# Kernel tuning notes

Hardware: AMD Instinct MI355X
Metric: run time of the kernel (lower is better)

Reference implementation:

```python
import jax, jax.numpy as jnp
import numpy as np

N_NODES = 50000
N_EDGES = 800000
HIDDEN = 128
NUM_GDL = 2


def setup_inputs() -> dict:
    key = jax.random.key(0)
    k0, k1, k2, k3, k4 = jax.random.split(key, 5)
    x = jax.random.normal(k0, (N_NODES, HIDDEN), dtype=jnp.float32)
    row = jax.random.randint(k1, (N_EDGES,), 0, N_NODES, dtype=jnp.int32)
    # ensure every node appears at least once as a target so degree >= 1
    col_tail = jax.random.randint(k2, (N_EDGES - N_NODES,), 0, N_NODES, dtype=jnp.int32)
    col = jnp.concatenate([jnp.arange(N_NODES, dtype=jnp.int32), col_tail])
    edge_index = jnp.stack([row, col], axis=0)  # [2, E]
    W1s = jax.random.normal(k3, (NUM_GDL, HIDDEN, HIDDEN), dtype=jnp.float32) / np.sqrt(HIDDEN).astype(np.float32)
    W2s = jax.random.normal(k4, (NUM_GDL, HIDDEN, 2 * HIDDEN), dtype=jnp.float32) / np.sqrt(2 * HIDDEN).astype(np.float32)
    biases = jnp.zeros((NUM_GDL, HIDDEN), dtype=jnp.float32)  # reset_parameters zeroes bias
    return {"x": x, "edge_index": edge_index, "W1s": W1s, "W2s": W2s, "biases": biases}


def reference(x, edge_index, W1s, W2s, biases):
    # eval mode: dropout is identity
    row, col = edge_index[0], edge_index[1]  # row = source j, col = target i
    n, d = x.shape
    deg = jax.ops.segment_sum(jnp.ones(row.shape[0], x.dtype), col, num_segments=n)
    norm = (1.0 / deg)[row]  # per-edge norm, indexed by row as in torch source
    for k in range(W1s.shape[0]):
        W1, W2, b = W1s[k], W2s[k], biases[k]
        # lin2(cat[x_i, x_j]) = x_i @ W2[:, :d].T + x_j @ W2[:, d:].T
        # precompute both node-level projections, then gather per edge (cheaper than per-edge GEMM)
        proj_i = x @ W2[:, :d].T  # [n, d]
        proj_j = x @ W2[:, d:].T  # [n, d]
        msg = norm[:, None] * (proj_i[col] + proj_j[row])  # [E, d]
        agg = jax.ops.segment_sum(msg, col, num_segments=n)  # scatter-add into targets
        out = x @ W1.T - agg + b
        x = jax.nn.gelu(out, approximate=False)  # torch nn.GELU default = exact erf
    return x
```

## Files before the change

### kernel.cpp

```cpp
#include <hip/hip_runtime.h>

#define N_NODES 50000
#define N_EDGES 800000
#define D 128
#define NBUCKET 196
#define CAP 8192
#define EPT 16
#define SCAT_BLOCKS 196
#define WCONV_BLOCKS 96
#define CAST_BLOCKS 6250
#define GEMM_TILES 391

typedef unsigned short ushort_t;
typedef __bf16 bf16x8 __attribute__((ext_vector_type(8)));
typedef float f32x4 __attribute__((ext_vector_type(4)));
typedef float f32x2 __attribute__((ext_vector_type(2)));

__device__ __forceinline__ ushort_t f2bf(float f) {
    unsigned u = __builtin_bit_cast(unsigned, f);
    u += 0x7FFFu + ((u >> 16) & 1u);
    return (ushort_t)(u >> 16);
}
__device__ __forceinline__ float bf2f(unsigned h16) {
    return __builtin_bit_cast(float, h16 << 16);
}

__global__ __launch_bounds__(256) void k_pre(const float* __restrict__ x, ushort_t* __restrict__ xb,
                                             const int* __restrict__ row, const int* __restrict__ col,
                                             int* __restrict__ bucket_cursor, int2* __restrict__ temp,
                                             const float* __restrict__ W1s, const float* __restrict__ W2s,
                                             ushort_t* __restrict__ Wb) {
    __shared__ int hist[NBUCKET];
    int b = blockIdx.x;
    if (b < SCAT_BLOCKS) {
        for (int t = threadIdx.x; t < NBUCKET; t += 256) hist[t] = 0;
        __syncthreads();
        int base = (b * 256 + threadIdx.x) * EPT;
        bool act = base < N_EDGES;
        int4 c[4], r[4];
        if (act) {
            #pragma unroll
            for (int q = 0; q < 4; ++q) c[q] = *(const int4*)(col + base + q * 4);
            #pragma unroll
            for (int q = 0; q < 4; ++q) r[q] = *(const int4*)(row + base + q * 4);
            #pragma unroll
            for (int q = 0; q < 4; ++q) {
                atomicAdd(&hist[c[q].x >> 8], 1); atomicAdd(&hist[c[q].y >> 8], 1);
                atomicAdd(&hist[c[q].z >> 8], 1); atomicAdd(&hist[c[q].w >> 8], 1);
            }
        }
        __syncthreads();
        for (int t = threadIdx.x; t < NBUCKET; t += 256) {
            int cnt = hist[t];
            hist[t] = cnt ? atomicAdd(&bucket_cursor[t], cnt) : 0;
        }
        __syncthreads();
        if (act) {
            #pragma unroll
            for (int q = 0; q < 4; ++q) {
                int cc[4] = { c[q].x, c[q].y, c[q].z, c[q].w };
                int rr[4] = { r[q].x, r[q].y, r[q].z, r[q].w };
                #pragma unroll
                for (int e = 0; e < 4; ++e) {
                    int bk = cc[e] >> 8;
                    int pos = atomicAdd(&hist[bk], 1);
                    temp[bk * CAP + pos] = make_int2(rr[e], cc[e]);
                }
            }
        }
    } else if (b < SCAT_BLOCKS + WCONV_BLOCKS) {
        int c = (b - SCAT_BLOCKS) * 256 + threadIdx.x;
        int k = c / 12288, rem = c % 12288;
        int mat = rem / 4096, rr = (rem % 4096) / 32, col4 = rem % 32;
        const float* src = (mat == 0)
            ? (W1s + k * 16384 + rr * 128 + col4 * 4)
            : (W2s + k * 32768 + rr * 256 + (mat == 2 ? 128 : 0) + col4 * 4);
        float4 v = *(const float4*)src;
        ushort_t tmp[4] = { f2bf(v.x), f2bf(v.y), f2bf(v.z), f2bf(v.w) };
        *(uint2*)(Wb + ((size_t)(k * 3 + mat)) * 16384 + rr * 128 + col4 * 4) = *(const uint2*)tmp;
    } else {
        int base = ((b - SCAT_BLOCKS - WCONV_BLOCKS) * 256 + threadIdx.x) * 4;
        if (base < N_NODES * D) {
            float4 v = *(const float4*)(x + base);
            ushort_t tmp[4] = { f2bf(v.x), f2bf(v.y), f2bf(v.z), f2bf(v.w) };
            *(uint2*)(xb + base) = *(const uint2*)tmp;
        }
    }
}

__device__ __forceinline__ void gemm_tile3(int m0,
                                           ushort_t (*As)[136], ushort_t (*Bs)[136],
                                           const ushort_t* __restrict__ xb,
                                           const ushort_t* __restrict__ Wl,
                                           const float* __restrict__ scl,
                                           ushort_t* __restrict__ Plb,
                                           ushort_t* __restrict__ Pi_,
                                           unsigned char* __restrict__ Pj8) {
    const int tid = threadIdx.x;
    #pragma unroll
    for (int it = 0; it < 8; ++it) {
        int c = tid + it * 256;
        int r = c >> 4, kc = c & 15;
        uint4 v = make_uint4(0, 0, 0, 0);
        int gm = m0 + r;
        if (gm < N_NODES) v = *(const uint4*)(xb + (size_t)gm * D + kc * 8);
        *(uint4*)&As[r][kc * 8] = v;
    }
    const int w = tid >> 6, lane = tid & 63, quad = lane >> 4, r16 = lane & 15;
    const int arow0 = w * 32 + r16, arow1 = arow0 + 16;
    #pragma unroll
    for (int y = 0; y < 3; ++y) {
        const ushort_t* Wmat = Wl + (size_t)y * 16384;
        #pragma unroll
        for (int it = 0; it < 8; ++it) {
            int c = tid + it * 256;
            int r = c >> 4, kc = c & 15;
            *(uint4*)&Bs[r][kc * 8] = *(const uint4*)(Wmat + r * 128 + kc * 8);
        }
        __syncthreads();
        f32x4 acc[2][8];
        #pragma unroll
        for (int mt = 0; mt < 2; ++mt)
            #pragma unroll
            for (int nt = 0; nt < 8; ++nt) acc[mt][nt] = (f32x4){0.f, 0.f, 0.f, 0.f};
        #pragma unroll
        for (int k0 = 0; k0 < 128; k0 += 32) {
            bf16x8 a0 = __builtin_bit_cast(bf16x8, *(const uint4*)&As[arow0][k0 + quad * 8]);
            bf16x8 a1 = __builtin_bit_cast(bf16x8, *(const uint4*)&As[arow1][k0 + quad * 8]);
            #pragma unroll
            for (int nt = 0; nt < 8; ++nt) {
                bf16x8 b = __builtin_bit_cast(bf16x8, *(const uint4*)&Bs[nt * 16 + r16][k0 + quad * 8]);
                acc[0][nt] = __builtin_amdgcn_mfma_f32_16x16x32_bf16(b, a0, acc[0][nt], 0, 0, 0);
                acc[1][nt] = __builtin_amdgcn_mfma_f32_16x16x32_bf16(b, a1, acc[1][nt], 0, 0, 0);
            }
        }
        #pragma unroll
        for (int mt = 0; mt < 2; ++mt) {
            int gm = m0 + w * 32 + mt * 16 + r16;
            if (gm >= N_NODES) continue;
            if (y < 2) {
                ushort_t* Outp = (y == 0) ? Plb : Pi_;
                #pragma unroll
                for (int nt = 0; nt < 8; ++nt) {
                    ushort_t tmp[4] = { f2bf(acc[mt][nt][0]), f2bf(acc[mt][nt][1]),
                                        f2bf(acc[mt][nt][2]), f2bf(acc[mt][nt][3]) };
                    *(uint2*)(Outp + (size_t)gm * D + nt * 16 + quad * 4) = *(const uint2*)tmp;
                }
            } else {
                float sc = scl ? scl[gm] : 1.0f;
                #pragma unroll
                for (int nt = 0; nt < 8; ++nt) {
                    int v = __builtin_amdgcn_cvt_pk_fp8_f32(acc[mt][nt][0] * sc, acc[mt][nt][1] * sc, 0, false);
                    v = __builtin_amdgcn_cvt_pk_fp8_f32(acc[mt][nt][2] * sc, acc[mt][nt][3] * sc, v, true);
                    *(unsigned*)(Pj8 + (size_t)gm * D + nt * 16 + quad * 4) = (unsigned)v;
                }
            }
        }
        if (y < 2) __syncthreads();
    }
}

__global__ __launch_bounds__(256) void k_bsort_gemm(const int2* __restrict__ temp,
                                                    const int* __restrict__ bucket_cursor,
                                                    int* __restrict__ csr, int* __restrict__ off,
                                                    int* __restrict__ deg, float* __restrict__ inv_deg,
                                                    const ushort_t* __restrict__ xb,
                                                    const ushort_t* __restrict__ Wb,
                                                    ushort_t* __restrict__ Plb,
                                                    ushort_t* __restrict__ Pi_,
                                                    unsigned char* __restrict__ Pj8) {
    __shared__ __align__(16) ushort_t As[128][136];
    __shared__ __align__(16) ushort_t Bs[128][136];
    __shared__ int hist[256];
    __shared__ int sm[256];
    if (blockIdx.x < NBUCKET) {
        int b = blockIdx.x, t = threadIdx.x;
        int cnt = bucket_cursor[b];
        sm[t] = (t < b) ? bucket_cursor[t] : 0;
        __syncthreads();
        for (int o = 1; o < 256; o <<= 1) {
            int add = (t >= o) ? sm[t - o] : 0;
            __syncthreads();
            sm[t] += add;
            __syncthreads();
        }
        int gbase = sm[255];
        int tbase = b * CAP;
        hist[t] = 0;
        __syncthreads();
        int i = t;
        for (; i + 768 < cnt; i += 1024) {
            int2 e0 = temp[tbase + i], e1 = temp[tbase + i + 256];
            int2 e2 = temp[tbase + i + 512], e3 = temp[tbase + i + 768];
            atomicAdd(&hist[e0.y & 255], 1); atomicAdd(&hist[e1.y & 255], 1);
            atomicAdd(&hist[e2.y & 255], 1); atomicAdd(&hist[e3.y & 255], 1);
        }
        for (; i < cnt; i += 256) atomicAdd(&hist[temp[tbase + i].y & 255], 1);
        __syncthreads();
        int c = hist[t];
        sm[t] = c;
        __syncthreads();
        for (int o = 1; o < 256; o <<= 1) {
            int add = (t >= o) ? sm[t - o] : 0;
            __syncthreads();
            sm[t] += add;
            __syncthreads();
        }
        int excl = sm[t] - c;
        int node = b * 256 + t;
        if (node < N_NODES) {
            off[node] = gbase + excl;
            deg[node] = c;
            inv_deg[node] = 1.0f / (float)c;
        }
        __syncthreads();
        hist[t] = gbase + excl;
        __syncthreads();
        i = t;
        for (; i + 768 < cnt; i += 1024) {
            int2 e0 = temp[tbase + i], e1 = temp[tbase + i + 256];
            int2 e2 = temp[tbase + i + 512], e3 = temp[tbase + i + 768];
            int p0 = atomicAdd(&hist[e0.y & 255], 1);
            int p1 = atomicAdd(&hist[e1.y & 255], 1);
            int p2 = atomicAdd(&hist[e2.y & 255], 1);
            int p3 = atomicAdd(&hist[e3.y & 255], 1);
            csr[p0] = e0.x; csr[p1] = e1.x; csr[p2] = e2.x; csr[p3] = e3.x;
        }
        for (; i < cnt; i += 256) {
            int2 e = temp[tbase + i];
            int p = atomicAdd(&hist[e.y & 255], 1);
            csr[p] = e.x;
        }
    } else {
        gemm_tile3((blockIdx.x - NBUCKET) * 128, As, Bs, xb, Wb, nullptr, Plb, Pi_, Pj8);
    }
}

__global__ __launch_bounds__(256) void k_gemm(const ushort_t* __restrict__ xb,
                                              const ushort_t* __restrict__ Wl,
                                              const float* __restrict__ inv_deg,
                                              ushort_t* __restrict__ Plb,
                                              ushort_t* __restrict__ Pi_,
                                              unsigned char* __restrict__ Pj8) {
    __shared__ __align__(16) ushort_t As[128][136];
    __shared__ __align__(16) ushort_t Bs[128][136];
    gemm_tile3(blockIdx.x * 128, As, Bs, xb, Wl, inv_deg, Plb, Pi_, Pj8);
}

__global__ __launch_bounds__(256) void k_agg(const ushort_t* __restrict__ Plb,
                                             const ushort_t* __restrict__ Pi_,
                                             const unsigned char* __restrict__ Pj8,
                                             const int* __restrict__ off,
                                             const int* __restrict__ deg,
                                             const int* __restrict__ csr,
                                             const float* __restrict__ inv_deg,
                                             const float* __restrict__ bias,
                                             float* __restrict__ s_arr,
                                             float* __restrict__ out_f32,
                                             ushort_t* __restrict__ out_bf16,
                                             int layer0) {
    int wv = __builtin_amdgcn_readfirstlane(threadIdx.x >> 6);
    int node = blockIdx.x * 4 + wv;
    if (node >= N_NODES) return;
    int lane = threadIdx.x & 63;
    unsigned ulin = *(const unsigned*)(Plb + (size_t)node * D + 2 * lane);
    unsigned upi  = *(const unsigned*)(Pi_ + (size_t)node * D + 2 * lane);
    float2 bv = *(const float2*)(bias + 2 * lane);
    float a0 = bf2f(ulin & 0xffffu) + bv.x;
    float a1 = bf2f(ulin >> 16)     + bv.y;
    float c0 = 0.f, c1 = 0.f, si;
    int e0 = off[node], ne = deg[node];
    int j = 0;
    if (layer0) {
        float sa = 0.f, sb = 0.f;
        for (; j + 16 <= ne; j += 16) {
            int sx[16];
            #pragma unroll
            for (int t = 0; t < 16; ++t) sx[t] = csr[e0 + j + t];
            unsigned u[16];
            #pragma unroll
            for (int t = 0; t < 16; ++t) u[t] = *(const ushort_t*)(Pj8 + (size_t)sx[t] * D + 2 * lane);
            float dv[16];
            #pragma unroll
            for (int t = 0; t < 16; ++t) dv[t] = inv_deg[sx[t]];
            #pragma unroll
            for (int t = 0; t < 16; t += 2) {
                f32x2 f0 = __builtin_amdgcn_cvt_pk_f32_fp8((int)u[t], false);
                f32x2 f1 = __builtin_amdgcn_cvt_pk_f32_fp8((int)u[t + 1], false);
                sa += dv[t]; sb += dv[t + 1];
                a0 -= dv[t] * f0[0];  c0 += dv[t + 1] * f1[0];
                a1 -= dv[t] * f0[1];  c1 += dv[t + 1] * f1[1];
            }
        }
        for (; j + 4 <= ne; j += 4) {
            int s0 = csr[e0 + j], s1 = csr[e0 + j + 1], s2 = csr[e0 + j + 2], s3 = csr[e0 + j + 3];
            unsigned u0 = *(const ushort_t*)(Pj8 + (size_t)s0 * D + 2 * lane);
            unsigned u1 = *(const ushort_t*)(Pj8 + (size_t)s1 * D + 2 * lane);
            unsigned u2 = *(const ushort_t*)(Pj8 + (size_t)s2 * D + 2 * lane);
            unsigned u3 = *(const ushort_t*)(Pj8 + (size_t)s3 * D + 2 * lane);
            float d0 = inv_deg[s0], d1 = inv_deg[s1], d2 = inv_deg[s2], d3 = inv_deg[s3];
            f32x2 f0 = __builtin_amdgcn_cvt_pk_f32_fp8((int)u0, false);
            f32x2 f1 = __builtin_amdgcn_cvt_pk_f32_fp8((int)u1, false);
            f32x2 f2 = __builtin_amdgcn_cvt_pk_f32_fp8((int)u2, false);
            f32x2 f3 = __builtin_amdgcn_cvt_pk_f32_fp8((int)u3, false);
            sa += d0 + d2; sb += d1 + d3;
            a0 -= d0 * f0[0] + d1 * f1[0];  c0 += d2 * f2[0] + d3 * f3[0];
            a1 -= d0 * f0[1] + d1 * f1[1];  c1 += d2 * f2[1] + d3 * f3[1];
        }
        for (; j < ne; ++j) {
            int s0 = csr[e0 + j];
            unsigned u0 = *(const ushort_t*)(Pj8 + (size_t)s0 * D + 2 * lane);
            float d0 = inv_deg[s0];
            f32x2 f0 = __builtin_amdgcn_cvt_pk_f32_fp8((int)u0, false);
            sa += d0;
            a0 -= d0 * f0[0];
            a1 -= d0 * f0[1];
        }
        si = sa + sb;
        if (lane == 0) s_arr[node] = si;
    } else {
        si = s_arr[node];
        for (; j + 16 <= ne; j += 16) {
            int sx[16];
            #pragma unroll
            for (int t = 0; t < 16; ++t) sx[t] = csr[e0 + j + t];
            unsigned u[16];
            #pragma unroll
            for (int t = 0; t < 16; ++t) u[t] = *(const ushort_t*)(Pj8 + (size_t)sx[t] * D + 2 * lane);
            #pragma unroll
            for (int t = 0; t < 16; t += 2) {
                f32x2 f0 = __builtin_amdgcn_cvt_pk_f32_fp8((int)u[t], false);
                f32x2 f1 = __builtin_amdgcn_cvt_pk_f32_fp8((int)u[t + 1], false);
                a0 -= f0[0];  c0 += f1[0];
                a1 -= f0[1];  c1 += f1[1];
            }
        }
        for (; j + 4 <= ne; j += 4) {
            int s0 = csr[e0 + j], s1 = csr[e0 + j + 1], s2 = csr[e0 + j + 2], s3 = csr[e0 + j + 3];
            unsigned u0 = *(const ushort_t*)(Pj8 + (size_t)s0 * D + 2 * lane);
            unsigned u1 = *(const ushort_t*)(Pj8 + (size_t)s1 * D + 2 * lane);
            unsigned u2 = *(const ushort_t*)(Pj8 + (size_t)s2 * D + 2 * lane);
            unsigned u3 = *(const ushort_t*)(Pj8 + (size_t)s3 * D + 2 * lane);
            f32x2 f0 = __builtin_amdgcn_cvt_pk_f32_fp8((int)u0, false);
            f32x2 f1 = __builtin_amdgcn_cvt_pk_f32_fp8((int)u1, false);
            f32x2 f2 = __builtin_amdgcn_cvt_pk_f32_fp8((int)u2, false);
            f32x2 f3 = __builtin_amdgcn_cvt_pk_f32_fp8((int)u3, false);
            a0 -= f0[0] + f1[0];  c0 += f2[0] + f3[0];
            a1 -= f0[1] + f1[1];  c1 += f2[1] + f3[1];
        }
        for (; j < ne; ++j) {
            int s0 = csr[e0 + j];
            unsigned u0 = *(const ushort_t*)(Pj8 + (size_t)s0 * D + 2 * lane);
            f32x2 f0 = __builtin_amdgcn_cvt_pk_f32_fp8((int)u0, false);
            a0 -= f0[0];
            a1 -= f0[1];
        }
    }
    a0 -= c0 + si * bf2f(upi & 0xffffu);
    a1 -= c1 + si * bf2f(upi >> 16);
    float g0 = 0.5f * a0 * (1.0f + erff(a0 * 0.70710678118654752440f));
    float g1 = 0.5f * a1 * (1.0f + erff(a1 * 0.70710678118654752440f));
    if (layer0) {
        ushort_t tmp[2] = { f2bf(g0), f2bf(g1) };
        *(unsigned*)(out_bf16 + (size_t)node * D + 2 * lane) = *(const unsigned*)tmp;
    } else {
        *(float2*)(out_f32 + (size_t)node * D + 2 * lane) = make_float2(g0, g1);
    }
}

extern "C" void kernel_launch(void* const* d_in, const int* in_sizes, int n_in,
                              void* d_out, int out_size, void* d_ws, size_t ws_size,
                              hipStream_t stream) {
    const float* x      = (const float*)d_in[0];
    const int*   ei     = (const int*)d_in[1];
    const int*   rowp   = ei;
    const int*   colp   = ei + N_EDGES;
    const float* W1s    = (const float*)d_in[2];
    const float* W2s    = (const float*)d_in[3];
    const float* biases = (const float*)d_in[4];
    float* out = (float*)d_out;

    char* ws = (char*)d_ws;
    size_t o = 0;
    auto carve = [&](size_t bytes) -> void* {
        void* p = ws + o;
        o = (o + bytes + 255) & ~(size_t)255;
        return p;
    };
    int*           bucket_cursor = (int*)carve(NBUCKET * 4);
    int*           deg     = (int*)carve(N_NODES * 4);
    float*         inv_deg = (float*)carve(N_NODES * 4);
    int*           off     = (int*)carve(N_NODES * 4);
    float*         s_arr   = (float*)carve(N_NODES * 4);
    int*           csr     = (int*)carve(N_EDGES * 4);
    int2*          temp    = (int2*)carve((size_t)NBUCKET * CAP * 8);
    ushort_t*      xb      = (ushort_t*)carve((size_t)N_NODES * D * 2);
    ushort_t*      Wb      = (ushort_t*)carve((size_t)2 * 3 * 16384 * 2);
    ushort_t*      Plb     = (ushort_t*)carve((size_t)N_NODES * D * 2);
    ushort_t*      Pi_     = (ushort_t*)carve((size_t)N_NODES * D * 2);
    unsigned char* Pj8     = (unsigned char*)carve((size_t)N_NODES * D);
    if (o > ws_size) return;

    hipMemsetAsync(bucket_cursor, 0, NBUCKET * 4, stream);

    k_pre<<<SCAT_BLOCKS + WCONV_BLOCKS + CAST_BLOCKS, 256, 0, stream>>>(x, xb, rowp, colp,
                                                                        bucket_cursor, temp,
                                                                        W1s, W2s, Wb);
    k_bsort_gemm<<<NBUCKET + GEMM_TILES, 256, 0, stream>>>(temp, bucket_cursor, csr, off,
                                                           deg, inv_deg, xb, Wb, Plb, Pi_, Pj8);

    const int AB = (N_NODES + 3) / 4;
    k_agg<<<AB, 256, 0, stream>>>(Plb, Pi_, Pj8, off, deg, csr, inv_deg, biases, s_arr,
                                  nullptr, xb, 1);
    k_gemm<<<GEMM_TILES, 256, 0, stream>>>(xb, Wb + (size_t)3 * 16384, inv_deg, Plb, Pi_, Pj8);
    k_agg<<<AB, 256, 0, stream>>>(Plb, Pi_, Pj8, off, deg, csr, inv_deg, biases + 128, s_arr,
                                  out, nullptr, 0);
}
```

Measured before the change: 206.1 us.

## Fuse x cast into GEMM, shrink CSR to 16-bit, widen agg gathers

```diff
diff --git a/kernel.cpp b/kernel.cpp
--- a/kernel.cpp
+++ b/kernel.cpp
@@ -8,7 +8,6 @@
 #define EPT 16
 #define SCAT_BLOCKS 196
 #define WCONV_BLOCKS 96
-#define CAST_BLOCKS 6250
 #define GEMM_TILES 391
 
 typedef unsigned short ushort_t;
@@ -25,9 +24,8 @@
     return __builtin_bit_cast(float, h16 << 16);
 }
 
-__global__ __launch_bounds__(256) void k_pre(const float* __restrict__ x, ushort_t* __restrict__ xb,
-                                             const int* __restrict__ row, const int* __restrict__ col,
-                                             int* __restrict__ bucket_cursor, int2* __restrict__ temp,
+__global__ __launch_bounds__(256) void k_pre(const int* __restrict__ row, const int* __restrict__ col,
+                                             int* __restrict__ bucket_cursor, unsigned* __restrict__ temp,
                                              const float* __restrict__ W1s, const float* __restrict__ W2s,
                                              ushort_t* __restrict__ Wb) {
     __shared__ int hist[NBUCKET];
@@ -64,11 +62,11 @@
                 for (int e = 0; e < 4; ++e) {
                     int bk = cc[e] >> 8;
                     int pos = atomicAdd(&hist[bk], 1);
-                    temp[bk * CAP + pos] = make_int2(rr[e], cc[e]);
+                    temp[bk * CAP + pos] = (unsigned)rr[e] | ((unsigned)(cc[e] & 255) << 16);
                 }
             }
         }
-    } else if (b < SCAT_BLOCKS + WCONV_BLOCKS) {
+    } else {
         int c = (b - SCAT_BLOCKS) * 256 + threadIdx.x;
         int k = c / 12288, rem = c % 12288;
         int mat = rem / 4096, rr = (rem % 4096) / 32, col4 = rem % 32;
@@ -78,33 +76,48 @@
         float4 v = *(const float4*)src;
         ushort_t tmp[4] = { f2bf(v.x), f2bf(v.y), f2bf(v.z), f2bf(v.w) };
         *(uint2*)(Wb + ((size_t)(k * 3 + mat)) * 16384 + rr * 128 + col4 * 4) = *(const uint2*)tmp;
-    } else {
-        int base = ((b - SCAT_BLOCKS - WCONV_BLOCKS) * 256 + threadIdx.x) * 4;
-        if (base < N_NODES * D) {
-            float4 v = *(const float4*)(x + base);
-            ushort_t tmp[4] = { f2bf(v.x), f2bf(v.y), f2bf(v.z), f2bf(v.w) };
-            *(uint2*)(xb + base) = *(const uint2*)tmp;
-        }
-    }
-}
-
+    }
+}
+
+template<bool AF32>
 __device__ __forceinline__ void gemm_tile3(int m0,
                                            ushort_t (*As)[136], ushort_t (*Bs)[136],
-                                           const ushort_t* __restrict__ xb,
+                                           const void* __restrict__ xsrc,
                                            const ushort_t* __restrict__ Wl,
                                            const float* __restrict__ scl,
                                            ushort_t* __restrict__ Plb,
                                            ushort_t* __restrict__ Pi_,
                                            unsigned char* __restrict__ Pj8) {
     const int tid = threadIdx.x;
-    #pragma unroll
-    for (int it = 0; it < 8; ++it) {
-        int c = tid + it * 256;
-        int r = c >> 4, kc = c & 15;
-        uint4 v = make_uint4(0, 0, 0, 0);
-        int gm = m0 + r;
-        if (gm < N_NODES) v = *(const uint4*)(xb + (size_t)gm * D + kc * 8);
-        *(uint4*)&As[r][kc * 8] = v;
+    if constexpr (AF32) {
+        const float* xf = (const float*)xsrc;
+        #pragma unroll
+        for (int it = 0; it < 8; ++it) {
+            int c = tid + it * 256;
+            int r = c >> 4, kc = c & 15;
+            uint4 v = make_uint4(0, 0, 0, 0);
+            int gm = m0 + r;
+            if (gm < N_NODES) {
+                float4 p0 = *(const float4*)(xf + (size_t)gm * D + kc * 8);
+                float4 p1 = *(const float4*)(xf + (size_t)gm * D + kc * 8 + 4);
+                ushort_t __attribute__((aligned(16))) tmp[8] =
+                    { f2bf(p0.x), f2bf(p0.y), f2bf(p0.z), f2bf(p0.w),
+                      f2bf(p1.x), f2bf(p1.y), f2bf(p1.z), f2bf(p1.w) };
+                v = *(const uint4*)tmp;
+            }
+            *(uint4*)&As[r][kc * 8] = v;
+        }
+    } else {
+        const ushort_t* xb = (const ushort_t*)xsrc;
+        #pragma unroll
+        for (int it = 0; it < 8; ++it) {
+            int c = tid + it * 256;
+            int r = c >> 4, kc = c & 15;
+            uint4 v = make_uint4(0, 0, 0, 0);
+            int gm = m0 + r;
+            if (gm < N_NODES) v = *(const uint4*)(xb + (size_t)gm * D + kc * 8);
+            *(uint4*)&As[r][kc * 8] = v;
+        }
     }
     const int w = tid >> 6, lane = tid & 63, quad = lane >> 4, r16 = lane & 15;
     const int arow0 = w * 32 + r16, arow1 = arow0 + 16;
@@ -160,11 +173,11 @@
     }
 }
 
-__global__ __launch_bounds__(256) void k_bsort_gemm(const int2* __restrict__ temp,
+__global__ __launch_bounds__(256) void k_bsort_gemm(const unsigned* __restrict__ temp,
                                                     const int* __restrict__ bucket_cursor,
-                                                    int* __restrict__ csr, int* __restrict__ off,
+                                                    ushort_t* __restrict__ csr, int* __restrict__ off,
                                                     int* __restrict__ deg, float* __restrict__ inv_deg,
-                                                    const ushort_t* __restrict__ xb,
+                                                    const float* __restrict__ xf,
                                                     const ushort_t* __restrict__ Wb,
                                                     ushort_t* __restrict__ Plb,
                                                     ushort_t* __restrict__ Pi_,
@@ -190,12 +203,12 @@
         __syncthreads();
         int i = t;
         for (; i + 768 < cnt; i += 1024) {
-            int2 e0 = temp[tbase + i], e1 = temp[tbase + i + 256];
-            int2 e2 = temp[tbase + i + 512], e3 = temp[tbase + i + 768];
-            atomicAdd(&hist[e0.y & 255], 1); atomicAdd(&hist[e1.y & 255], 1);
-            atomicAdd(&hist[e2.y & 255], 1); atomicAdd(&hist[e3.y & 255], 1);
-        }
-        for (; i < cnt; i += 256) atomicAdd(&hist[temp[tbase + i].y & 255], 1);
+            unsigned e0 = temp[tbase + i], e1 = temp[tbase + i + 256];
+            unsigned e2 = temp[tbase + i + 512], e3 = temp[tbase + i + 768];
+            atomicAdd(&hist[e0 >> 16], 1); atomicAdd(&hist[e1 >> 16], 1);
+            atomicAdd(&hist[e2 >> 16], 1); atomicAdd(&hist[e3 >> 16], 1);
+        }
+        for (; i < cnt; i += 256) atomicAdd(&hist[temp[tbase + i] >> 16], 1);
         __syncthreads();
         int c = hist[t];
         sm[t] = c;
@@ -218,21 +231,22 @@
         __syncthreads();
         i = t;
         for (; i + 768 < cnt; i += 1024) {
-            int2 e0 = temp[tbase + i], e1 = temp[tbase + i + 256];
-            int2 e2 = temp[tbase + i + 512], e3 = temp[tbase + i + 768];
-            int p0 = atomicAdd(&hist[e0.y & 255], 1);
-            int p1 = atomicAdd(&hist[e1.y & 255], 1);
-            int p2 = atomicAdd(&hist[e2.y & 255], 1);
-            int p3 = atomicAdd(&hist[e3.y & 255], 1);
-            csr[p0] = e0.x; csr[p1] = e1.x; csr[p2] = e2.x; csr[p3] = e3.x;
+            unsigned e0 = temp[tbase + i], e1 = temp[tbase + i + 256];
+            unsigned e2 = temp[tbase + i + 512], e3 = temp[tbase + i + 768];
+            int p0 = atomicAdd(&hist[e0 >> 16], 1);
+            int p1 = atomicAdd(&hist[e1 >> 16], 1);
+            int p2 = atomicAdd(&hist[e2 >> 16], 1);
+            int p3 = atomicAdd(&hist[e3 >> 16], 1);
+            csr[p0] = (ushort_t)e0; csr[p1] = (ushort_t)e1;
+            csr[p2] = (ushort_t)e2; csr[p3] = (ushort_t)e3;
         }
         for (; i < cnt; i += 256) {
-            int2 e = temp[tbase + i];
-            int p = atomicAdd(&hist[e.y & 255], 1);
-            csr[p] = e.x;
-        }
-    } else {
-        gemm_tile3((blockIdx.x - NBUCKET) * 128, As, Bs, xb, Wb, nullptr, Plb, Pi_, Pj8);
+            unsigned e = temp[tbase + i];
+            int p = atomicAdd(&hist[e >> 16], 1);
+            csr[p] = (ushort_t)e;
+        }
+    } else {
+        gemm_tile3<true>((blockIdx.x - NBUCKET) * 128, As, Bs, xf, Wb, nullptr, Plb, Pi_, Pj8);
     }
 }
 
@@ -244,7 +258,7 @@
                                               unsigned char* __restrict__ Pj8) {
     __shared__ __align__(16) ushort_t As[128][136];
     __shared__ __align__(16) ushort_t Bs[128][136];
-    gemm_tile3(blockIdx.x * 128, As, Bs, xb, Wl, inv_deg, Plb, Pi_, Pj8);
+    gemm_tile3<false>(blockIdx.x * 128, As, Bs, xb, Wl, inv_deg, Plb, Pi_, Pj8);
 }
 
 __global__ __launch_bounds__(256) void k_agg(const ushort_t* __restrict__ Plb,
@@ -252,7 +266,7 @@
                                              const unsigned char* __restrict__ Pj8,
                                              const int* __restrict__ off,
                                              const int* __restrict__ deg,
-                                             const int* __restrict__ csr,
+                                             const ushort_t* __restrict__ csr,
                                              const float* __restrict__ inv_deg,
                                              const float* __restrict__ bias,
                                              float* __restrict__ s_arr,
@@ -262,109 +276,146 @@
     int wv = __builtin_amdgcn_readfirstlane(threadIdx.x >> 6);
     int node = blockIdx.x * 4 + wv;
     if (node >= N_NODES) return;
-    int lane = threadIdx.x & 63;
-    unsigned ulin = *(const unsigned*)(Plb + (size_t)node * D + 2 * lane);
-    unsigned upi  = *(const unsigned*)(Pi_ + (size_t)node * D + 2 * lane);
-    float2 bv = *(const float2*)(bias + 2 * lane);
-    float a0 = bf2f(ulin & 0xffffu) + bv.x;
-    float a1 = bf2f(ulin >> 16)     + bv.y;
-    float c0 = 0.f, c1 = 0.f, si;
-    int e0 = off[node], ne = deg[node];
+    const int lane = threadIdx.x & 63;
+    const int g = lane >> 4;
+    const int q8 = lane & 15;
+    const int eoff = 8 * q8 + 2 * g;
+    unsigned ulin = *(const unsigned*)(Plb + (size_t)node * D + eoff);
+    unsigned upi  = *(const unsigned*)(Pi_ + (size_t)node * D + eoff);
+    float2 bv = *(const float2*)(bias + eoff);
+    float su[8];
+    #pragma unroll
+    for (int k = 0; k < 8; ++k) su[k] = 0.f;
+    float sd = 0.f;
+    const int e0 = off[node], ne = deg[node];
     int j = 0;
     if (layer0) {
-        float sa = 0.f, sb = 0.f;
         for (; j + 16 <= ne; j += 16) {
-            int sx[16];
-            #pragma unroll
-            for (int t = 0; t < 16; ++t) sx[t] = csr[e0 + j + t];
-            unsigned u[16];
-            #pragma unroll
-            for (int t = 0; t < 16; ++t) u[t] = *(const ushort_t*)(Pj8 + (size_t)sx[t] * D + 2 * lane);
-            float dv[16];
-            #pragma unroll
-            for (int t = 0; t < 16; ++t) dv[t] = inv_deg[sx[t]];
-            #pragma unroll
-            for (int t = 0; t < 16; t += 2) {
-                f32x2 f0 = __builtin_amdgcn_cvt_pk_f32_fp8((int)u[t], false);
-                f32x2 f1 = __builtin_amdgcn_cvt_pk_f32_fp8((int)u[t + 1], false);
-                sa += dv[t]; sb += dv[t + 1];
-                a0 -= dv[t] * f0[0];  c0 += dv[t + 1] * f1[0];
-                a1 -= dv[t] * f0[1];  c1 += dv[t + 1] * f1[1];
+            int sx[4];
+            #pragma unroll
+            for (int t = 0; t < 4; ++t) sx[t] = csr[e0 + j + 4 * t + g];
+            uint2 u[4];
+            #pragma unroll
+            for (int t = 0; t < 4; ++t) u[t] = *(const uint2*)(Pj8 + (size_t)sx[t] * D + 8 * q8);
+            float dv[4];
+            #pragma unroll
+            for (int t = 0; t < 4; ++t) dv[t] = inv_deg[sx[t]];
+            #pragma unroll
+            for (int t = 0; t < 4; ++t) {
+                f32x2 f0 = __builtin_amdgcn_cvt_pk_f32_fp8((int)u[t].x, false);
+                f32x2 f1 = __builtin_amdgcn_cvt_pk_f32_fp8((int)u[t].x, true);
+                f32x2 f2 = __builtin_amdgcn_cvt_pk_f32_fp8((int)u[t].y, false);
+                f32x2 f3 = __builtin_amdgcn_cvt_pk_f32_fp8((int)u[t].y, true);
+                sd += dv[t];
+                su[0] += dv[t] * f0[0]; su[1] += dv[t] * f0[1];
+                su[2] += dv[t] * f1[0]; su[3] += dv[t] * f1[1];
+                su[4] += dv[t] * f2[0]; su[5] += dv[t] * f2[1];
+                su[6] += dv[t] * f3[0]; su[7] += dv[t] * f3[1];
             }
         }
         for (; j + 4 <= ne; j += 4) {
-            int s0 = csr[e0 + j], s1 = csr[e0 + j + 1], s2 = csr[e0 + j + 2], s3 = csr[e0 + j + 3];
-            unsigned u0 = *(const ushort_t*)(Pj8 + (size_t)s0 * D + 2 * lane);
-            unsigned u1 = *(const ushort_t*)(Pj8 + (size_t)s1 * D + 2 * lane);
-            unsigned u2 = *(const ushort_t*)(Pj8 + (size_t)s2 * D + 2 * lane);
-            unsigned u3 = *(const ushort_t*)(Pj8 + (size_t)s3 * D + 2 * lane);
-            float d0 = inv_deg[s0], d1 = inv_deg[s1], d2 = inv_deg[s2], d3 = inv_deg[s3];
-            f32x2 f0 = __builtin_amdgcn_cvt_pk_f32_fp8((int)u0, false);
-            f32x2 f1 = __builtin_amdgcn_cvt_pk_f32_fp8((int)u1, false);
-            f32x2 f2 = __builtin_amdgcn_cvt_pk_f32_fp8((int)u2, false);
-            f32x2 f3 = __builtin_amdgcn_cvt_pk_f32_fp8((int)u3, false);
-            sa += d0 + d2; sb += d1 + d3;
-            a0 -= d0 * f0[0] + d1 * f1[0];  c0 += d2 * f2[0] + d3 * f3[0];
-            a1 -= d0 * f0[1] + d1 * f1[1];  c1 += d2 * f2[1] + d3 * f3[1];
-        }
-        for (; j < ne; ++j) {
-            int s0 = csr[e0 + j];
-            unsigned u0 = *(const ushort_t*)(Pj8 + (size_t)s0 * D + 2 * lane);
-            float d0 = inv_deg[s0];
-            f32x2 f0 = __builtin_amdgcn_cvt_pk_f32_fp8((int)u0, false);
-            sa += d0;
-            a0 -= d0 * f0[0];
-            a1 -= d0 * f0[1];
-        }
-        si = sa + sb;
+            int sx = csr[e0 + j + g];
+            uint2 u = *(const uint2*)(Pj8 + (size_t)sx * D + 8 * q8);
+            float dv = inv_deg[sx];
+            f32x2 f0 = __builtin_amdgcn_cvt_pk_f32_fp8((int)u.x, false);
+            f32x2 f1 = __builtin_amdgcn_cvt_pk_f32_fp8((int)u.x, true);
+            f32x2 f2 = __builtin_amdgcn_cvt_pk_f32_fp8((int)u.y, false);
+            f32x2 f3 = __builtin_amdgcn_cvt_pk_f32_fp8((int)u.y, true);
+            sd += dv;
+            su[0] += dv * f0[0]; su[1] += dv * f0[1];
+            su[2] += dv * f1[0]; su[3] += dv * f1[1];
+            su[4] += dv * f2[0]; su[5] += dv * f2[1];
+            su[6] += dv * f3[0]; su[7] += dv * f3[1];
+        }
+        if (j < ne) {
+            int r = ne - j;
+            int gi = (g < r) ? g : (r - 1);
+            int sx = csr[e0 + j + gi];
+            uint2 u = *(const uint2*)(Pj8 + (size_t)sx * D + 8 * q8);
+            float dv = (g < r) ? inv_deg[sx] : 0.f;
+            f32x2 f0 = __builtin_amdgcn_cvt_pk_f32_fp8((int)u.x, false);
+            f32x2 f1 = __builtin_amdgcn_cvt_pk_f32_fp8((int)u.x, true);
+            f32x2 f2 = __builtin_amdgcn_cvt_pk_f32_fp8((int)u.y, false);
+            f32x2 f3 = __builtin_amdgcn_cvt_pk_f32_fp8((int)u.y, true);
+            sd += dv;
+            su[0] += dv * f0[0]; su[1] += dv * f0[1];
+            su[2] += dv * f1[0]; su[3] += dv * f1[1];
+            su[4] += dv * f2[0]; su[5] += dv * f2[1];
+            su[6] += dv * f3[0]; su[7] += dv * f3[1];
+        }
+    } else {
+        for (; j + 16 <= ne; j += 16) {
+            int sx[4];
+            #pragma unroll
+            for (int t = 0; t < 4; ++t) sx[t] = csr[e0 + j + 4 * t + g];
+            uint2 u[4];
+            #pragma unroll
+            for (int t = 0; t < 4; ++t) u[t] = *(const uint2*)(Pj8 + (size_t)sx[t] * D + 8 * q8);
+            #pragma unroll
+            for (int t = 0; t < 4; ++t) {
+                f32x2 f0 = __builtin_amdgcn_cvt_pk_f32_fp8((int)u[t].x, false);
+                f32x2 f1 = __builtin_amdgcn_cvt_pk_f32_fp8((int)u[t].x, true);
+                f32x2 f2 = __builtin_amdgcn_cvt_pk_f32_fp8((int)u[t].y, false);
+                f32x2 f3 = __builtin_amdgcn_cvt_pk_f32_fp8((int)u[t].y, true);
+                su[0] += f0[0]; su[1] += f0[1];
+                su[2] += f1[0]; su[3] += f1[1];
+                su[4] += f2[0]; su[5] += f2[1];
+                su[6] += f3[0]; su[7] += f3[1];
+            }
+        }
+        for (; j + 4 <= ne; j += 4) {
+            int sx = csr[e0 + j + g];
+            uint2 u = *(const uint2*)(Pj8 + (size_t)sx * D + 8 * q8);
+            f32x2 f0 = __builtin_amdgcn_cvt_pk_f32_fp8((int)u.x, false);
+            f32x2 f1 = __builtin_amdgcn_cvt_pk_f32_fp8((int)u.x, true);
+            f32x2 f2 = __builtin_amdgcn_cvt_pk_f32_fp8((int)u.y, false);
+            f32x2 f3 = __builtin_amdgcn_cvt_pk_f32_fp8((int)u.y, true);
+            su[0] += f0[0]; su[1] += f0[1];
+            su[2] += f1[0]; su[3] += f1[1];
+            su[4] += f2[0]; su[5] += f2[1];
+            su[6] += f3[0]; su[7] += f3[1];
+        }
+        if (j < ne) {
+            int r = ne - j;
+            int gi = (g < r) ? g : (r - 1);
+            int sx = csr[e0 + j + gi];
+            uint2 u = *(const uint2*)(Pj8 + (size_t)sx * D + 8 * q8);
+            float wt = (g < r) ? 1.f : 0.f;
+            f32x2 f0 = __builtin_amdgcn_cvt_pk_f32_fp8((int)u.x, false);
+            f32x2 f1 = __builtin_amdgcn_cvt_pk_f32_fp8((int)u.x, true);
+            f32x2 f2 = __builtin_amdgcn_cvt_pk_f32_fp8((int)u.y, false);
+            f32x2 f3 = __builtin_amdgcn_cvt_pk_f32_fp8((int)u.y, true);
+            su[0] += wt * f0[0]; su[1] += wt * f0[1];
+            su[2] += wt * f1[0]; su[3] += wt * f1[1];
+            su[4] += wt * f2[0]; su[5] += wt * f2[1];
+            su[6] += wt * f3[0]; su[7] += wt * f3[1];
+        }
+    }
+    #pragma unroll
+    for (int k = 0; k < 8; ++k) {
+        su[k] += __shfl_xor(su[k], 16);
+        su[k] += __shfl_xor(su[k], 32);
+    }
+    float si;
+    if (layer0) {
+        sd += __shfl_xor(sd, 16);
+        sd += __shfl_xor(sd, 32);
+        si = sd;
         if (lane == 0) s_arr[node] = si;
     } else {
         si = s_arr[node];
-        for (; j + 16 <= ne; j += 16) {
-            int sx[16];
-            #pragma unroll
-            for (int t = 0; t < 16; ++t) sx[t] = csr[e0 + j + t];
-            unsigned u[16];
-            #pragma unroll
-            for (int t = 0; t < 16; ++t) u[t] = *(const ushort_t*)(Pj8 + (size_t)sx[t] * D + 2 * lane);
-            #pragma unroll
-            for (int t = 0; t < 16; t += 2) {
-                f32x2 f0 = __builtin_amdgcn_cvt_pk_f32_fp8((int)u[t], false);
-                f32x2 f1 = __builtin_amdgcn_cvt_pk_f32_fp8((int)u[t + 1], false);
-                a0 -= f0[0];  c0 += f1[0];
-                a1 -= f0[1];  c1 += f1[1];
-            }
-        }
-        for (; j + 4 <= ne; j += 4) {
-            int s0 = csr[e0 + j], s1 = csr[e0 + j + 1], s2 = csr[e0 + j + 2], s3 = csr[e0 + j + 3];
-            unsigned u0 = *(const ushort_t*)(Pj8 + (size_t)s0 * D + 2 * lane);
-            unsigned u1 = *(const ushort_t*)(Pj8 + (size_t)s1 * D + 2 * lane);
-            unsigned u2 = *(const ushort_t*)(Pj8 + (size_t)s2 * D + 2 * lane);
-            unsigned u3 = *(const ushort_t*)(Pj8 + (size_t)s3 * D + 2 * lane);
-            f32x2 f0 = __builtin_amdgcn_cvt_pk_f32_fp8((int)u0, false);
-            f32x2 f1 = __builtin_amdgcn_cvt_pk_f32_fp8((int)u1, false);
-            f32x2 f2 = __builtin_amdgcn_cvt_pk_f32_fp8((int)u2, false);
-            f32x2 f3 = __builtin_amdgcn_cvt_pk_f32_fp8((int)u3, false);
-            a0 -= f0[0] + f1[0];  c0 += f2[0] + f3[0];
-            a1 -= f0[1] + f1[1];  c1 += f2[1] + f3[1];
-        }
-        for (; j < ne; ++j) {
-            int s0 = csr[e0 + j];
-            unsigned u0 = *(const ushort_t*)(Pj8 + (size_t)s0 * D + 2 * lane);
-            f32x2 f0 = __builtin_amdgcn_cvt_pk_f32_fp8((int)u0, false);
-            a0 -= f0[0];
-            a1 -= f0[1];
-        }
-    }
-    a0 -= c0 + si * bf2f(upi & 0xffffu);
-    a1 -= c1 + si * bf2f(upi >> 16);
+    }
+    float t0 = (g < 2) ? ((g == 0) ? su[0] : su[2]) : ((g == 2) ? su[4] : su[6]);
+    float t1 = (g < 2) ? ((g == 0) ? su[1] : su[3]) : ((g == 2) ? su[5] : su[7]);
+    float a0 = bf2f(ulin & 0xffffu) + bv.x - si * bf2f(upi & 0xffffu) - t0;
+    float a1 = bf2f(ulin >> 16)     + bv.y - si * bf2f(upi >> 16)     - t1;
     float g0 = 0.5f * a0 * (1.0f + erff(a0 * 0.70710678118654752440f));
     float g1 = 0.5f * a1 * (1.0f + erff(a1 * 0.70710678118654752440f));
     if (layer0) {
         ushort_t tmp[2] = { f2bf(g0), f2bf(g1) };
-        *(unsigned*)(out_bf16 + (size_t)node * D + 2 * lane) = *(const unsigned*)tmp;
-    } else {
-        *(float2*)(out_f32 + (size_t)node * D + 2 * lane) = make_float2(g0, g1);
+        *(unsigned*)(out_bf16 + (size_t)node * D + eoff) = *(const unsigned*)tmp;
+    } else {
+        *(float2*)(out_f32 + (size_t)node * D + eoff) = make_float2(g0, g1);
     }
 }
 
@@ -392,8 +443,8 @@
     float*         inv_deg = (float*)carve(N_NODES * 4);
     int*           off     = (int*)carve(N_NODES * 4);
     float*         s_arr   = (float*)carve(N_NODES * 4);
-    int*           csr     = (int*)carve(N_EDGES * 4);
-    int2*          temp    = (int2*)carve((size_t)NBUCKET * CAP * 8);
+    ushort_t*      csr     = (ushort_t*)carve((size_t)N_EDGES * 2);
+    unsigned*      temp    = (unsigned*)carve((size_t)NBUCKET * CAP * 4);
     ushort_t*      xb      = (ushort_t*)carve((size_t)N_NODES * D * 2);
     ushort_t*      Wb      = (ushort_t*)carve((size_t)2 * 3 * 16384 * 2);
     ushort_t*      Plb     = (ushort_t*)carve((size_t)N_NODES * D * 2);
@@ -403,11 +454,10 @@
 
     hipMemsetAsync(bucket_cursor, 0, NBUCKET * 4, stream);
 
-    k_pre<<<SCAT_BLOCKS + WCONV_BLOCKS + CAST_BLOCKS, 256, 0, stream>>>(x, xb, rowp, colp,
-                                                                        bucket_cursor, temp,
-                                                                        W1s, W2s, Wb);
+    k_pre<<<SCAT_BLOCKS + WCONV_BLOCKS, 256, 0, stream>>>(rowp, colp, bucket_cursor, temp,
+                                                          W1s, W2s, Wb);
     k_bsort_gemm<<<NBUCKET + GEMM_TILES, 256, 0, stream>>>(temp, bucket_cursor, csr, off,
-                                                           deg, inv_deg, xb, Wb, Plb, Pi_, Pj8);
+                                                           deg, inv_deg, x, Wb, Plb, Pi_, Pj8);
 
     const int AB = (N_NODES + 3) / 4;
     k_agg<<<AB, 256, 0, stream>>>(Plb, Pi_, Pj8, off, deg, csr, inv_deg, biases, s_arr,
```

Result: no change. 205.7 us (-0.2%).
